# Kernel optimization log

Hardware: AMD Instinct MI355X
Metric: run time of the kernel (lower is better)

Reference implementation:

```python
import jax, jax.numpy as jnp
import numpy as np

B, C, D, H, W = 4, 256, 16, 16, 16
INTER = C // 8  # 32


def setup_inputs() -> dict:
    key = jax.random.key(0)
    ks = jax.random.split(key, 8)
    return {
        "x": jax.random.normal(ks[0], (B, C, D, H, W), dtype=jnp.float32),
        "Wq": jax.random.normal(ks[1], (INTER, C), dtype=jnp.float32) * 0.05,
        "bq": jax.random.normal(ks[2], (INTER,), dtype=jnp.float32) * 0.05,
        "Wk": jax.random.normal(ks[3], (INTER, C), dtype=jnp.float32) * 0.05,
        "bk": jax.random.normal(ks[4], (INTER,), dtype=jnp.float32) * 0.05,
        "Wv": jax.random.normal(ks[5], (C, C), dtype=jnp.float32) * 0.05,
        "bv": jax.random.normal(ks[6], (C,), dtype=jnp.float32) * 0.05,
        "gamma": jax.random.normal(ks[7], (1,), dtype=jnp.float32),
    }


def reference(x, Wq, bq, Wk, bk, Wv, bv, gamma):
    b, c, d, h, w = x.shape
    n = d * h * w
    xf = x.reshape(b, c, n)  # [B, C, N]
    # 1x1 Conv3d == pointwise channel projection
    q = jnp.einsum("oc,bcn->bon", Wq, xf) + bq[None, :, None]  # [B, inter, N]
    k = jnp.einsum("oc,bcn->bon", Wk, xf) + bk[None, :, None]  # [B, inter, N]
    v = jnp.einsum("oc,bcn->bon", Wv, xf) + bv[None, :, None]  # [B, C, N]
    scale = float(q.shape[1]) ** 0.5
    # attn[b, i, j] = <q[:, i], k[:, j]>
    attn = jax.nn.softmax(jnp.einsum("bci,bcj->bij", q, k) / scale, axis=-1)
    # out[b, c, i] = sum_j v[b, c, j] * attn[b, i, j]
    out = jnp.einsum("bcj,bij->bci", v, attn).reshape(b, c, d, h, w)
    return gamma[0] * out + x
```

## Files before the change

kernel.cpp:

```cpp
#include <hip/hip_runtime.h>

#define B_ 4
#define C_ 256
#define N_ 4096
#define INTER_ 32

typedef __attribute__((ext_vector_type(8))) short short8;
typedef __attribute__((ext_vector_type(4))) float f32x4;
typedef __attribute__((ext_vector_type(16))) float f32x16;
typedef __attribute__((ext_vector_type(4))) unsigned int u32x4;

#define TILEB 18432
#define NSTG  (8 * TILEB)

static __device__ __forceinline__ unsigned short f2bf(float f) {
    unsigned int u = __builtin_bit_cast(unsigned int, f);
    u += 0x7fff + ((u >> 16) & 1);
    return (unsigned short)(u >> 16);
}

static __device__ __forceinline__ unsigned int cvtpk(float lo, float hi) {
    unsigned int r;
    asm("v_cvt_pk_bf16_f32 %0, %1, %2" : "=v"(r) : "v"(lo), "v"(hi));
    return r;
}

static __device__ __forceinline__ void pl32swap(unsigned int& a, unsigned int& b) {
    asm("v_permlane32_swap_b32 %0, %1" : "+v"(a), "+v"(b));
}

static __device__ __forceinline__ void gload16(const void* g, void* l) {
    __builtin_amdgcn_global_load_lds(
        (const __attribute__((address_space(1))) void*)g,
        (__attribute__((address_space(3))) void*)l, 16, 0, 0);
}

__global__ __launch_bounds__(256) void prep_kernel(
    const float* __restrict__ Wq, const float* __restrict__ Wk,
    const float* __restrict__ Wv, unsigned short* __restrict__ wb)
{
    int i = blockIdx.x * 256 + threadIdx.x;
    int row = i >> 8, col = i & 255;
    float v;
    if (row < 32)      v = Wq[row * 256 + col];
    else if (row < 64) v = Wk[(row - 32) * 256 + col];
    else               v = Wv[(row - 64) * 256 + col];
    wb[i] = f2bf(v);
}

__global__ __launch_bounds__(256) void qkv_kernel(
    const float* __restrict__ x, const unsigned short* __restrict__ wb,
    const float* __restrict__ bq, const float* __restrict__ bk,
    const float* __restrict__ bv,
    unsigned short* __restrict__ qb, unsigned short* __restrict__ kfrag,
    unsigned short* __restrict__ vfrag)
{
    const int tid  = threadIdx.x;
    const int wave = tid >> 6;
    const int lane = tid & 63;
    const int l31  = lane & 31;
    const int h2   = lane >> 5;
    const int b    = blockIdx.x >> 6;
    const int n0   = (blockIdx.x & 63) * 64;

    __shared__ unsigned int xsh[64 * 129];

    {
        const float* xb = x + ((size_t)b * C_ + 64 * wave) * N_ + n0 + lane;
        unsigned int* dst = xsh + (size_t)lane * 129 + 32 * wave;
        #pragma unroll 8
        for (int s = 0; s < 32; ++s) {
            float v0 = xb[(size_t)(2 * s) * N_];
            float v1 = xb[(size_t)(2 * s + 1) * N_];
            dst[s] = (unsigned int)f2bf(v0) | ((unsigned int)f2bf(v1) << 16);
        }
    }
    __syncthreads();

    const float rs = 0.25504183f;

    #pragma unroll
    for (int u = 0; u < 5; ++u) {
        const int unit = wave + 4 * u;
        const int ch = unit >> 1;
        const int ns = unit & 1;
        const int ncol = n0 + 32 * ns + l31;
        const int jt = (n0 >> 5) + ns;

        const float* bias = (ch == 0) ? bq : (ch == 1) ? bk : (bv + (ch - 2) * 32);
        f32x16 acc;
        #pragma unroll
        for (int r = 0; r < 16; ++r)
            acc[r] = bias[(r & 3) + 8 * (r >> 2) + 4 * h2];

        const unsigned short* wrow = wb + ((size_t)(ch * 32 + l31)) * 256 + 8 * h2;
        const unsigned int*   xrow = xsh + (size_t)(32 * ns + l31) * 129 + 4 * h2;

        #pragma unroll
        for (int kk = 0; kk < 16; ++kk) {
            short8 wa = *reinterpret_cast<const short8*>(wrow + 16 * kk);
            short8 xf = *reinterpret_cast<const short8*>(xrow + 8 * kk);
            acc = __builtin_amdgcn_mfma_f32_32x32x16_bf16(wa, xf, acc, 0, 0, 0);
        }

        if (ch == 0) {
            unsigned short* dst = qb + ((size_t)b * N_ + ncol) * 32;
            #pragma unroll
            for (int q = 0; q < 4; ++q) {
                unsigned int w0 = (unsigned int)f2bf(acc[4 * q] * rs)
                                | ((unsigned int)f2bf(acc[4 * q + 1] * rs) << 16);
                unsigned int w1 = (unsigned int)f2bf(acc[4 * q + 2] * rs)
                                | ((unsigned int)f2bf(acc[4 * q + 3] * rs) << 16);
                unsigned int* p = reinterpret_cast<unsigned int*>(dst + 4 * h2 + 8 * q);
                p[0] = w0; p[1] = w1;
            }
        } else if (ch == 1) {
            unsigned short* kt = kfrag + ((size_t)b * 128 + jt) * 1024;
            #pragma unroll
            for (int r = 0; r < 16; ++r) {
                const int co = (r & 3) + 8 * (r >> 2) + 4 * h2;
                const int addr = ((co >> 4) << 9) + ((l31 + 32 * ((co >> 3) & 1)) << 3)
                               + (co & 7);
                kt[addr] = f2bf(acc[r]);
            }
        } else {
            const int g = ch - 2;
            unsigned short* vt_ = vfrag + (((size_t)b * 128 + jt) * 8 + g) * 1024;
            #pragma unroll
            for (int r = 0; r < 16; ++r) {
                const int co = (r & 3) + 8 * (r >> 2) + 4 * h2;
                const int addr = ((l31 >> 4) << 9) + ((co + 32 * ((l31 >> 3) & 1)) << 3)
                               + (l31 & 7);
                vt_[addr] = f2bf(acc[r]);
            }
        }
    }
}

__global__ __launch_bounds__(512) void attn_kernel(
    const unsigned short* __restrict__ qb, const unsigned short* __restrict__ kfrag,
    const unsigned short* __restrict__ vfrag,
    const float* __restrict__ x, const float* __restrict__ gamma,
    float* __restrict__ out)
{
    const int tid  = threadIdx.x;
    const int wave = tid >> 6;
    const int lane = tid & 63;
    const int l31  = lane & 31;
    const int h2   = lane >> 5;
    const int jq   = wave >> 1;
    const int qs   = wave & 1;

    const int bid  = blockIdx.x;
    const int xcd  = bid & 7;
    const int slot = bid >> 3;
    const int b    = xcd >> 1;
    const int ib   = slot * 2 + (xcd & 1);
    const int iq   = ib * 64 + 32 * qs;

    __shared__ char lds[NSTG];
    __shared__ float m_sh[8][32];
    __shared__ float l_sh[8][32];

    const unsigned short* vtb = vfrag + (size_t)b * 128 * 8192;
    const unsigned short* ktb = kfrag + (size_t)b * 128 * 1024;

    char* reg0 = lds + (jq * 2) * TILEB;
    char* reg1 = reg0 + TILEB;

    short8 qf0 = *reinterpret_cast<const short8*>(
        qb + ((size_t)b * N_ + iq + l31) * 32 + 8 * h2);
    short8 qf1 = *reinterpret_cast<const short8*>(
        qb + ((size_t)b * N_ + iq + l31) * 32 + 8 * h2 + 16);

    f32x16 acc[8];
    #pragma unroll
    for (int g = 0; g < 8; ++g)
        #pragma unroll
        for (int r = 0; r < 16; ++r) acc[g][r] = 0.f;

    float m_run = 0.f;
    float l_run = 0.f;
    const f32x16 z16 = {};

    {
        const int jtg = jq * 32;
        const char* vs = (const char*)(vtb + (size_t)jtg * 8192);
        if (qs == 0) {
            #pragma unroll
            for (int s2 = 0; s2 < 9; ++s2)
                gload16(vs + s2 * 1024 + lane * 16, reg0 + s2 * 1024);
        } else {
            #pragma unroll
            for (int s2 = 9; s2 < 16; ++s2)
                gload16(vs + s2 * 1024 + lane * 16, reg0 + s2 * 1024);
            const char* ks = (const char*)(ktb + (size_t)jtg * 1024);
            gload16(ks + lane * 16, reg0 + 16384);
            gload16(ks + 1024 + lane * 16, reg0 + 17408);
        }
    }
    __syncthreads();

    #pragma unroll 1
    for (int t = 0; t < 32; ++t) {
        char* cur = (t & 1) ? reg1 : reg0;
        char* nxt = (t & 1) ? reg0 : reg1;

        if (t < 31) {
            const int jtg = jq * 32 + t + 1;
            const char* vs = (const char*)(vtb + (size_t)jtg * 8192);
            if (qs == 0) {
                #pragma unroll
                for (int s2 = 0; s2 < 9; ++s2)
                    gload16(vs + s2 * 1024 + lane * 16, nxt + s2 * 1024);
            } else {
                #pragma unroll
                for (int s2 = 9; s2 < 16; ++s2)
                    gload16(vs + s2 * 1024 + lane * 16, nxt + s2 * 1024);
                const char* ks = (const char*)(ktb + (size_t)jtg * 1024);
                gload16(ks + lane * 16, nxt + 16384);
                gload16(ks + 1024 + lane * 16, nxt + 17408);
            }
        }

        const char* kt_ = cur + 16384;
        short8 ka0 = *reinterpret_cast<const short8*>(kt_ + lane * 16);
        short8 ka1 = *reinterpret_cast<const short8*>(kt_ + 1024 + lane * 16);
        f32x16 s = __builtin_amdgcn_mfma_f32_32x32x16_bf16(ka0, qf0, z16, 0, 0, 0);
        s = __builtin_amdgcn_mfma_f32_32x32x16_bf16(ka1, qf1, s, 0, 0, 0);

        float a0 = fmaxf(s[0], s[8]),  a1 = fmaxf(s[1], s[9]);
        float a2 = fmaxf(s[2], s[10]), a3 = fmaxf(s[3], s[11]);
        float a4 = fmaxf(s[4], s[12]), a5 = fmaxf(s[5], s[13]);
        float a6 = fmaxf(s[6], s[14]), a7 = fmaxf(s[7], s[15]);
        a0 = fmaxf(a0, a4); a1 = fmaxf(a1, a5); a2 = fmaxf(a2, a6); a3 = fmaxf(a3, a7);
        float smax = fmaxf(fmaxf(a0, a1), fmaxf(a2, a3));

        if (__any(smax > m_run + 8.0f)) {
            float sm2 = fmaxf(smax, __shfl_xor(smax, 32));
            float mnew = fmaxf(m_run, sm2);
            float corr = exp2f(m_run - mnew);
            m_run = mnew;
            l_run *= corr;
            #pragma unroll
            for (int g = 0; g < 8; ++g)
                #pragma unroll
                for (int r = 0; r < 16; ++r) acc[g][r] *= corr;
        }

        float p[16];
        float lsum = 0.f;
        #pragma unroll
        for (int r = 0; r < 16; ++r) { p[r] = exp2f(s[r] - m_run); lsum += p[r]; }
        l_run += lsum;

        unsigned int X0 = cvtpk(p[0],  p[1]),  X1 = cvtpk(p[2],  p[3]);
        unsigned int Y0 = cvtpk(p[4],  p[5]),  Y1 = cvtpk(p[6],  p[7]);
        unsigned int W0 = cvtpk(p[8],  p[9]),  W1 = cvtpk(p[10], p[11]);
        unsigned int V0 = cvtpk(p[12], p[13]), V1 = cvtpk(p[14], p[15]);
        pl32swap(X0, Y0); pl32swap(X1, Y1);
        pl32swap(W0, V0); pl32swap(W1, V1);
        short8 pb0 = __builtin_bit_cast(short8, u32x4{X0, X1, Y0, Y1});
        short8 pb1 = __builtin_bit_cast(short8, u32x4{W0, W1, V0, V1});

        __builtin_amdgcn_s_setprio(1);
        #pragma unroll
        for (int g = 0; g < 8; ++g) {
            short8 va0 = *reinterpret_cast<const short8*>(cur + g * 2048 + lane * 16);
            short8 va1 = *reinterpret_cast<const short8*>(cur + g * 2048 + 1024 + lane * 16);
            acc[g] = __builtin_amdgcn_mfma_f32_32x32x16_bf16(va0, pb0, acc[g], 0, 0, 0);
            acc[g] = __builtin_amdgcn_mfma_f32_32x32x16_bf16(va1, pb1, acc[g], 0, 0, 0);
        }
        __builtin_amdgcn_s_setprio(0);

        __syncthreads();
    }

    float l_tot = l_run + __shfl_xor(l_run, 32);
    if (lane < 32) { m_sh[wave][lane] = m_run; l_sh[wave][lane] = l_tot; }
    __syncthreads();

    float M = -1e30f, L = 0.f;
    #pragma unroll
    for (int w2 = 0; w2 < 4; ++w2) M = fmaxf(M, m_sh[w2 * 2 + qs][l31]);
    #pragma unroll
    for (int w2 = 0; w2 < 4; ++w2)
        L += exp2f(m_sh[w2 * 2 + qs][l31] - M) * l_sh[w2 * 2 + qs][l31];
    const float wgt = exp2f(m_run - M);
    #pragma unroll
    for (int g = 0; g < 8; ++g)
        #pragma unroll
        for (int r = 0; r < 16; ++r) acc[g][r] *= wgt;

    if (jq >= 2) {
        f32x4* Dr = (f32x4*)(lds + ((jq - 2) * 2 + qs) * 32768);
        #pragma unroll
        for (int g = 0; g < 8; ++g)
            #pragma unroll
            for (int r4 = 0; r4 < 4; ++r4) {
                f32x4 tv;
                #pragma unroll
                for (int e = 0; e < 4; ++e) tv[e] = acc[g][4 * r4 + e];
                Dr[(g * 4 + r4) * 64 + lane] = tv;
            }
    }
    __syncthreads();
    if (jq < 2) {
        const f32x4* Dr = (const f32x4*)(lds + (jq * 2 + qs) * 32768);
        #pragma unroll
        for (int g = 0; g < 8; ++g)
            #pragma unroll
            for (int r4 = 0; r4 < 4; ++r4) {
                f32x4 tv = Dr[(g * 4 + r4) * 64 + lane];
                #pragma unroll
                for (int e = 0; e < 4; ++e) acc[g][4 * r4 + e] += tv[e];
            }
    }
    __syncthreads();
    if (jq == 1) {
        f32x4* Dr = (f32x4*)(lds + (2 + qs) * 32768);
        #pragma unroll
        for (int g = 0; g < 8; ++g)
            #pragma unroll
            for (int r4 = 0; r4 < 4; ++r4) {
                f32x4 tv;
                #pragma unroll
                for (int e = 0; e < 4; ++e) tv[e] = acc[g][4 * r4 + e];
                Dr[(g * 4 + r4) * 64 + lane] = tv;
            }
    }
    __syncthreads();
    if (jq == 0) {
        const f32x4* Dr = (const f32x4*)(lds + (2 + qs) * 32768);
        f32x4* Dw = (f32x4*)(lds + qs * 32768);
        #pragma unroll
        for (int g = 0; g < 8; ++g)
            #pragma unroll
            for (int r4 = 0; r4 < 4; ++r4) {
                f32x4 tv = Dr[(g * 4 + r4) * 64 + lane];
                #pragma unroll
                for (int e = 0; e < 4; ++e) tv[e] += acc[g][4 * r4 + e];
                Dw[(g * 4 + r4) * 64 + lane] = tv;
            }
    }
    __syncthreads();

    const float gma  = gamma[0];
    const float invL = 1.f / L;
    const f32x4* Ds = (const f32x4*)(lds + qs * 32768);
    const int i = iq + l31;
    #pragma unroll
    for (int gi = 0; gi < 2; ++gi) {
        const int g = jq * 2 + gi;
        #pragma unroll
        for (int r4 = 0; r4 < 4; ++r4) {
            f32x4 v = Ds[(g * 4 + r4) * 64 + lane];
            #pragma unroll
            for (int e = 0; e < 4; ++e) {
                const int c = 32 * g + e + 8 * r4 + 4 * h2;
                const size_t off = ((size_t)b * C_ + c) * N_ + i;
                out[off] = gma * v[e] * invL + x[off];
            }
        }
    }
}

extern "C" void kernel_launch(void* const* d_in, const int* in_sizes, int n_in,
                              void* d_out, int out_size, void* d_ws, size_t ws_size,
                              hipStream_t stream) {
    const float* x     = (const float*)d_in[0];
    const float* Wq    = (const float*)d_in[1];
    const float* bq    = (const float*)d_in[2];
    const float* Wk    = (const float*)d_in[3];
    const float* bk    = (const float*)d_in[4];
    const float* Wv    = (const float*)d_in[5];
    const float* bv    = (const float*)d_in[6];
    const float* gamma = (const float*)d_in[7];
    float* out = (float*)d_out;

    unsigned short* ws = (unsigned short*)d_ws;
    unsigned short* qb    = ws;
    unsigned short* kfrag = qb + (size_t)B_ * N_ * INTER_;
    unsigned short* vfrag = kfrag + (size_t)B_ * 128 * 1024;
    unsigned short* wb    = vfrag + (size_t)B_ * 128 * 8192;

    prep_kernel<<<dim3(320), 256, 0, stream>>>(Wq, Wk, Wv, wb);
    qkv_kernel<<<dim3(B_ * (N_ / 64)), 256, 0, stream>>>(
        x, wb, bq, bk, bv, qb, kfrag, vfrag);
    attn_kernel<<<dim3(256), 512, 0, stream>>>(
        qb, kfrag, vfrag, x, gamma, out);
}
```

Before: 89.97 us.

## Restructure attention into 4-wave blocks with per-wave single-buffer staging

The attention kernel moves from 512-thread blocks to 256-thread blocks (two per CU, 512 blocks). Each wave now owns one 32-row query tile and a private key split. Every wave stages its own full V/K tile into a single private LDS buffer and pulls the whole tile into registers before issuing the next prefetch. This replaces the block-wide __syncthreads per iteration with per-wave waitcnt. The final cross-wave reduction becomes a two-phase LDS sum. The aim is to remove block-level barriers and paired-wave coupling, at the cost of higher register pressure from holding 16 V fragments and possible exposure of load latency, since only one buffer is used per wave.

```diff
diff --git a/kernel.cpp b/kernel.cpp
--- a/kernel.cpp
+++ b/kernel.cpp
@@ -11,7 +11,6 @@
 typedef __attribute__((ext_vector_type(4))) unsigned int u32x4;
 
 #define TILEB 18432
-#define NSTG  (8 * TILEB)
 
 static __device__ __forceinline__ unsigned short f2bf(float f) {
     unsigned int u = __builtin_bit_cast(unsigned int, f);
@@ -137,7 +136,7 @@
     }
 }
 
-__global__ __launch_bounds__(512) void attn_kernel(
+__global__ __launch_bounds__(256, 2) void attn_kernel(
     const unsigned short* __restrict__ qb, const unsigned short* __restrict__ kfrag,
     const unsigned short* __restrict__ vfrag,
     const float* __restrict__ x, const float* __restrict__ gamma,
@@ -148,30 +147,36 @@
     const int lane = tid & 63;
     const int l31  = lane & 31;
     const int h2   = lane >> 5;
-    const int jq   = wave >> 1;
-    const int qs   = wave & 1;
 
     const int bid  = blockIdx.x;
     const int xcd  = bid & 7;
     const int slot = bid >> 3;
     const int b    = xcd >> 1;
-    const int ib   = slot * 2 + (xcd & 1);
-    const int iq   = ib * 64 + 32 * qs;
-
-    __shared__ char lds[NSTG];
-    __shared__ float m_sh[8][32];
-    __shared__ float l_sh[8][32];
+    const int ib   = (xcd & 1) * 64 + slot;
+    const int i0   = ib * 32;
+
+    __shared__ char lds[4 * TILEB];
+    __shared__ float m_sh[4][32];
+    __shared__ float l_sh[4][32];
 
     const unsigned short* vtb = vfrag + (size_t)b * 128 * 8192;
     const unsigned short* ktb = kfrag + (size_t)b * 128 * 1024;
 
-    char* reg0 = lds + (jq * 2) * TILEB;
-    char* reg1 = reg0 + TILEB;
-
-    short8 qf0 = *reinterpret_cast<const short8*>(
-        qb + ((size_t)b * N_ + iq + l31) * 32 + 8 * h2);
-    short8 qf1 = *reinterpret_cast<const short8*>(
-        qb + ((size_t)b * N_ + iq + l31) * 32 + 8 * h2 + 16);
+    char* buf = lds + wave * TILEB;
+
+#define STAGE(jtg_) do {                                                      \
+        const char* vs_ = (const char*)(vtb + (size_t)(jtg_) * 8192);         \
+        _Pragma("unroll")                                                     \
+        for (int s2_ = 0; s2_ < 16; ++s2_)                                    \
+            gload16(vs_ + s2_ * 1024 + lane * 16, buf + s2_ * 1024);          \
+        const char* ks_ = (const char*)(ktb + (size_t)(jtg_) * 1024);         \
+        gload16(ks_ + lane * 16, buf + 16384);                                \
+        gload16(ks_ + 1024 + lane * 16, buf + 17408);                         \
+    } while (0)
+
+    const unsigned short* qbase = qb + ((size_t)b * N_ + i0 + l31) * 32 + 8 * h2;
+    short8 qf0 = *reinterpret_cast<const short8*>(qbase);
+    short8 qf1 = *reinterpret_cast<const short8*>(qbase + 16);
 
     f32x16 acc[8];
     #pragma unroll
@@ -179,53 +184,28 @@
         #pragma unroll
         for (int r = 0; r < 16; ++r) acc[g][r] = 0.f;
 
-    float m_run = 0.f;
-    float l_run = 0.f;
+    float m_run = 0.f, l_run = 0.f;
     const f32x16 z16 = {};
 
-    {
-        const int jtg = jq * 32;
-        const char* vs = (const char*)(vtb + (size_t)jtg * 8192);
-        if (qs == 0) {
-            #pragma unroll
-            for (int s2 = 0; s2 < 9; ++s2)
-                gload16(vs + s2 * 1024 + lane * 16, reg0 + s2 * 1024);
-        } else {
-            #pragma unroll
-            for (int s2 = 9; s2 < 16; ++s2)
-                gload16(vs + s2 * 1024 + lane * 16, reg0 + s2 * 1024);
-            const char* ks = (const char*)(ktb + (size_t)jtg * 1024);
-            gload16(ks + lane * 16, reg0 + 16384);
-            gload16(ks + 1024 + lane * 16, reg0 + 17408);
-        }
-    }
-    __syncthreads();
+    STAGE(wave * 32);
+    asm volatile("s_waitcnt vmcnt(0)" ::: "memory");
+    __builtin_amdgcn_sched_barrier(0);
 
     #pragma unroll 1
     for (int t = 0; t < 32; ++t) {
-        char* cur = (t & 1) ? reg1 : reg0;
-        char* nxt = (t & 1) ? reg0 : reg1;
-
-        if (t < 31) {
-            const int jtg = jq * 32 + t + 1;
-            const char* vs = (const char*)(vtb + (size_t)jtg * 8192);
-            if (qs == 0) {
-                #pragma unroll
-                for (int s2 = 0; s2 < 9; ++s2)
-                    gload16(vs + s2 * 1024 + lane * 16, nxt + s2 * 1024);
-            } else {
-                #pragma unroll
-                for (int s2 = 9; s2 < 16; ++s2)
-                    gload16(vs + s2 * 1024 + lane * 16, nxt + s2 * 1024);
-                const char* ks = (const char*)(ktb + (size_t)jtg * 1024);
-                gload16(ks + lane * 16, nxt + 16384);
-                gload16(ks + 1024 + lane * 16, nxt + 17408);
-            }
-        }
-
-        const char* kt_ = cur + 16384;
-        short8 ka0 = *reinterpret_cast<const short8*>(kt_ + lane * 16);
-        short8 ka1 = *reinterpret_cast<const short8*>(kt_ + 1024 + lane * 16);
+        short8 ka0 = *reinterpret_cast<const short8*>(buf + 16384 + lane * 16);
+        short8 ka1 = *reinterpret_cast<const short8*>(buf + 17408 + lane * 16);
+        short8 va[16];
+        #pragma unroll
+        for (int g = 0; g < 8; ++g) {
+            va[2 * g]     = *reinterpret_cast<const short8*>(buf + g * 2048 + lane * 16);
+            va[2 * g + 1] = *reinterpret_cast<const short8*>(buf + g * 2048 + 1024 + lane * 16);
+        }
+        asm volatile("s_waitcnt lgkmcnt(0)" ::: "memory");
+        __builtin_amdgcn_sched_barrier(0);
+
+        if (t < 31) STAGE(wave * 32 + t + 1);
+
         f32x16 s = __builtin_amdgcn_mfma_f32_32x32x16_bf16(ka0, qf0, z16, 0, 0, 0);
         s = __builtin_amdgcn_mfma_f32_32x32x16_bf16(ka1, qf1, s, 0, 0, 0);
 
@@ -266,15 +246,15 @@
         __builtin_amdgcn_s_setprio(1);
         #pragma unroll
         for (int g = 0; g < 8; ++g) {
-            short8 va0 = *reinterpret_cast<const short8*>(cur + g * 2048 + lane * 16);
-            short8 va1 = *reinterpret_cast<const short8*>(cur + g * 2048 + 1024 + lane * 16);
-            acc[g] = __builtin_amdgcn_mfma_f32_32x32x16_bf16(va0, pb0, acc[g], 0, 0, 0);
-            acc[g] = __builtin_amdgcn_mfma_f32_32x32x16_bf16(va1, pb1, acc[g], 0, 0, 0);
+            acc[g] = __builtin_amdgcn_mfma_f32_32x32x16_bf16(va[2 * g],     pb0, acc[g], 0, 0, 0);
+            acc[g] = __builtin_amdgcn_mfma_f32_32x32x16_bf16(va[2 * g + 1], pb1, acc[g], 0, 0, 0);
         }
         __builtin_amdgcn_s_setprio(0);
 
-        __syncthreads();
+        asm volatile("s_waitcnt vmcnt(0)" ::: "memory");
+        __builtin_amdgcn_sched_barrier(0);
     }
+#undef STAGE
 
     float l_tot = l_run + __shfl_xor(l_run, 32);
     if (lane < 32) { m_sh[wave][lane] = m_run; l_sh[wave][lane] = l_tot; }
@@ -282,84 +262,48 @@
 
     float M = -1e30f, L = 0.f;
     #pragma unroll
-    for (int w2 = 0; w2 < 4; ++w2) M = fmaxf(M, m_sh[w2 * 2 + qs][l31]);
-    #pragma unroll
-    for (int w2 = 0; w2 < 4; ++w2)
-        L += exp2f(m_sh[w2 * 2 + qs][l31] - M) * l_sh[w2 * 2 + qs][l31];
+    for (int w = 0; w < 4; ++w) M = fmaxf(M, m_sh[w][l31]);
+    #pragma unroll
+    for (int w = 0; w < 4; ++w) L += exp2f(m_sh[w][l31] - M) * l_sh[w][l31];
     const float wgt = exp2f(m_run - M);
     #pragma unroll
     for (int g = 0; g < 8; ++g)
         #pragma unroll
         for (int r = 0; r < 16; ++r) acc[g][r] *= wgt;
 
-    if (jq >= 2) {
-        f32x4* Dr = (f32x4*)(lds + ((jq - 2) * 2 + qs) * 32768);
-        #pragma unroll
-        for (int g = 0; g < 8; ++g)
+    const float gma  = gamma[0];
+    const float invL = 1.f / L;
+    f32x4* D = reinterpret_cast<f32x4*>(lds);
+
+    #pragma unroll
+    for (int ph = 0; ph < 2; ++ph) {
+        const int gbase = ph * 4;
+        __syncthreads();
+        #pragma unroll
+        for (int gl = 0; gl < 4; ++gl) {
+            const int g = gbase + gl;
             #pragma unroll
             for (int r4 = 0; r4 < 4; ++r4) {
                 f32x4 tv;
                 #pragma unroll
                 for (int e = 0; e < 4; ++e) tv[e] = acc[g][4 * r4 + e];
-                Dr[(g * 4 + r4) * 64 + lane] = tv;
-            }
-    }
-    __syncthreads();
-    if (jq < 2) {
-        const f32x4* Dr = (const f32x4*)(lds + (jq * 2 + qs) * 32768);
-        #pragma unroll
-        for (int g = 0; g < 8; ++g)
-            #pragma unroll
-            for (int r4 = 0; r4 < 4; ++r4) {
-                f32x4 tv = Dr[(g * 4 + r4) * 64 + lane];
-                #pragma unroll
-                for (int e = 0; e < 4; ++e) acc[g][4 * r4 + e] += tv[e];
-            }
-    }
-    __syncthreads();
-    if (jq == 1) {
-        f32x4* Dr = (f32x4*)(lds + (2 + qs) * 32768);
-        #pragma unroll
-        for (int g = 0; g < 8; ++g)
-            #pragma unroll
-            for (int r4 = 0; r4 < 4; ++r4) {
-                f32x4 tv;
-                #pragma unroll
-                for (int e = 0; e < 4; ++e) tv[e] = acc[g][4 * r4 + e];
-                Dr[(g * 4 + r4) * 64 + lane] = tv;
-            }
-    }
-    __syncthreads();
-    if (jq == 0) {
-        const f32x4* Dr = (const f32x4*)(lds + (2 + qs) * 32768);
-        f32x4* Dw = (f32x4*)(lds + qs * 32768);
-        #pragma unroll
-        for (int g = 0; g < 8; ++g)
-            #pragma unroll
-            for (int r4 = 0; r4 < 4; ++r4) {
-                f32x4 tv = Dr[(g * 4 + r4) * 64 + lane];
-                #pragma unroll
-                for (int e = 0; e < 4; ++e) tv[e] += acc[g][4 * r4 + e];
-                Dw[(g * 4 + r4) * 64 + lane] = tv;
-            }
-    }
-    __syncthreads();
-
-    const float gma  = gamma[0];
-    const float invL = 1.f / L;
-    const f32x4* Ds = (const f32x4*)(lds + qs * 32768);
-    const int i = iq + l31;
-    #pragma unroll
-    for (int gi = 0; gi < 2; ++gi) {
-        const int g = jq * 2 + gi;
+                D[((wave * 4 + gl) * 4 + r4) * 64 + lane] = tv;
+            }
+        }
+        __syncthreads();
+        const int g = gbase + wave;
         #pragma unroll
         for (int r4 = 0; r4 < 4; ++r4) {
-            f32x4 v = Ds[(g * 4 + r4) * 64 + lane];
+            f32x4 s0 = D[((0 * 4 + wave) * 4 + r4) * 64 + lane];
+            f32x4 s1 = D[((1 * 4 + wave) * 4 + r4) * 64 + lane];
+            f32x4 s2 = D[((2 * 4 + wave) * 4 + r4) * 64 + lane];
+            f32x4 s3 = D[((3 * 4 + wave) * 4 + r4) * 64 + lane];
             #pragma unroll
             for (int e = 0; e < 4; ++e) {
+                const float v = s0[e] + s1[e] + s2[e] + s3[e];
                 const int c = 32 * g + e + 8 * r4 + 4 * h2;
-                const size_t off = ((size_t)b * C_ + c) * N_ + i;
-                out[off] = gma * v[e] * invL + x[off];
+                const size_t off = ((size_t)b * C_ + c) * N_ + i0 + l31;
+                out[off] = gma * v * invL + x[off];
             }
         }
     }
@@ -387,6 +331,6 @@
     prep_kernel<<<dim3(320), 256, 0, stream>>>(Wq, Wk, Wv, wb);
     qkv_kernel<<<dim3(B_ * (N_ / 64)), 256, 0, stream>>>(
         x, wb, bq, bk, bv, qb, kfrag, vfrag);
-    attn_kernel<<<dim3(256), 512, 0, stream>>>(
+    attn_kernel<<<dim3(512), 256, 0, stream>>>(
         qb, kfrag, vfrag, x, gamma, out);
 }
```

Result: slower. 97.72 us (+8.6%).
